# Kernel tuning notes

Hardware: AMD Instinct MI355X
Metric: run time of the kernel (lower is better)

## Reference

```python
import jax, jax.numpy as jnp
import numpy as np

EDGE_WEIGHT = 5.0
LOW, HIGH = 50.0, 150.0          # cv2.Canny thresholds
TG22 = 0.4142135623730951        # tan(22.5 deg)
TG67 = 2.414213562373095         # tan(67.5 deg)


def _conv3(x, k):
    # x: [B,H,W], k: [3,3]; replicate border like cv2.Sobel in Canny
    xp = jnp.pad(x, ((0, 0), (1, 1), (1, 1)), mode='edge')[:, None]
    return jax.lax.conv_general_dilated(xp, k[None, None], (1, 1), 'VALID')[:, 0]


def _dilate(x, k):
    # binary max-pool dilation, zero border (cv2.dilate on 0/255 images)
    return jax.lax.reduce_window(x, 0.0, jax.lax.max, (1, k, k), (1, 1, 1), 'SAME')


def _canny_edge_weight(mask):
    # mask: [B,H,W] float in [0,1] -> per-pixel BCE weight map [B,H,W]
    img = (mask > 0.5).astype(jnp.float32) * 255.0
    kx = jnp.array([[-1., 0., 1.], [-2., 0., 2.], [-1., 0., 1.]], jnp.float32)
    ky = jnp.array([[-1., -2., -1.], [0., 0., 0.], [1., 2., 1.]], jnp.float32)
    gx, gy = _conv3(img, kx), _conv3(img, ky)
    m = jnp.abs(gx) + jnp.abs(gy)  # L1 magnitude (cv2 default L2gradient=False)
    B, H, W = m.shape
    mp = jnp.pad(m, ((0, 0), (1, 1), (1, 1)))  # zero-pad for neighbor lookup
    left, right = mp[:, 1:-1, :-2], mp[:, 1:-1, 2:]
    up, down = mp[:, :-2, 1:-1], mp[:, 2:, 1:-1]
    ul, ur = mp[:, :-2, :-2], mp[:, :-2, 2:]
    dl, dr = mp[:, 2:, :-2], mp[:, 2:, 2:]
    ax, ay = jnp.abs(gx), jnp.abs(gy)
    horiz = ay < ax * TG22
    vert = ay > ax * TG67
    sign_diff = (gx * gy) < 0
    # quantized-direction non-maximum suppression (cv2 tie-breaking: > prev, >= next)
    keep = jnp.where(horiz, (m > left) & (m >= right),
           jnp.where(vert, (m > up) & (m >= down),
           jnp.where(sign_diff, (m > ur) & (m >= dl),
                               (m > ul) & (m >= dr))))
    interior = jnp.zeros((H, W), bool).at[1:-1, 1:-1].set(True)
    cand = keep & (m > LOW) & interior
    weak = cand.astype(jnp.float32)
    strong = (cand & (m > HIGH)).astype(jnp.float32)

    # hysteresis: grow strong edges through weak candidates (8-connectivity)
    def cond(c):
        return c[1]

    def body(c):
        s, _ = c
        ns = jnp.maximum(s, jnp.minimum(weak, _dilate(s, 3)))
        return ns, jnp.any(ns != s)

    strong, _ = jax.lax.while_loop(cond, body, (strong, jnp.array(True)))
    edge_zone = _dilate(strong, 5)  # cv2.dilate(edges, ones(5,5))
    return jnp.where(edge_zone > 0, EDGE_WEIGHT, 1.0)


def setup_inputs() -> dict:
    key = jax.random.key(0)
    k1, k2 = jax.random.split(key)
    B, C, H, W = 16, 1, 1024, 1024
    pred = jax.random.uniform(k1, (B, C, H, W), jnp.float32) * 0.998 + 0.001
    target = (jax.random.uniform(k2, (B, C, H, W), jnp.float32) > 0.7).astype(jnp.float32)
    return {"pred": pred, "target": target}


def reference(pred, target):
    # edge weights from GT mask (detached path, matches .cpu().numpy())
    w = _canny_edge_weight(jax.lax.stop_gradient(target[:, 0]))[:, None]  # [B,1,H,W]
    # BCELoss(reduction='none') with torch's log clamp at -100
    logp = jnp.clip(jnp.log(pred), -100.0)
    log1mp = jnp.clip(jnp.log1p(-pred), -100.0)
    bce = -(target * logp + (1.0 - target) * log1mp)
    return (bce * w).mean()
```

## Files before the change

### kernel.cpp

```cpp
#include <hip/hip_runtime.h>
#include <math.h>


typedef unsigned long long u64;
typedef unsigned int u32;
typedef unsigned short u16;

#define NT 256
#define H_IMG 1024
#define W_IMG 1024
#define WPR 32

constexpr u64 K1 = 0x1111111111111111ULL;
constexpr u64 K7 = 0x7777777777777777ULL;
constexpr u64 K8 = 0x8888888888888888ULL;

__device__ __forceinline__ u64 geq8(u64 x, u64 y) { return ((x | K8) - y) & K8; }
__device__ __forceinline__ u64 gt8(u64 x, u64 y) { return K8 & ~((y | K8) - x); }

__global__ __launch_bounds__(256)
void binarize_kernel(const float* __restrict__ target, u32* __restrict__ packed,
                     int nwords)
{
    int t = blockIdx.x * 256 + threadIdx.x;
    if (t >= nwords) return;
    const float4* src = (const float4*)target + (size_t)t * 8;
    u32 v = 0;
#pragma unroll
    for (int k = 0; k < 8; ++k) {
        float4 f = src[k];
        v |= (f.x > 0.5f ? 1u : 0u) << (4 * k);
        v |= (f.y > 0.5f ? 2u : 0u) << (4 * k);
        v |= (f.z > 0.5f ? 4u : 0u) << (4 * k);
        v |= (f.w > 0.5f ? 8u : 0u) << (4 * k);
    }
    packed[t] = v;
}

__global__ __launch_bounds__(NT)
void edge_loss_kernel(const float* __restrict__ pred,
                      const u32* __restrict__ packed,
                      float* __restrict__ partials)
{
    __shared__ u32 simg[72][11];
    __shared__ u64 mw[70][6];
    __shared__ u64 clw[70][6];
    __shared__ u16 ssw[68][5];
    __shared__ u64 hrow[68];
    __shared__ float wsum[NT / 64];

    const int tid = threadIdx.x;
    const int bz = blockIdx.z;
    const int r0 = blockIdx.y * 64;
    const int c0 = blockIdx.x * 64;
    const float* pimg = pred + (size_t)bz * H_IMG * W_IMG;
    const u32* pb = packed + (size_t)bz * H_IMG * WPR;
    const int W0 = c0 >> 5;

    for (int t = tid; t < 72; t += NT) {
        int r = r0 - 4 + t; r = r < 0 ? 0 : (r > H_IMG - 1 ? H_IMG - 1 : r);
        const u32* prow = pb + r * WPR;
        u32 Bw = prow[W0];
        u32 Cw = prow[W0 + 1];
        u32 Aw = (W0 > 0) ? prow[W0 - 1] : ((Bw & 1u) ? ~0u : 0u);
        u32 Dw = (W0 + 2 < WPR) ? prow[W0 + 2] : ((Cw >> 31) ? ~0u : 0u);
        u64 lo = (u64)(Aw >> 28) | ((u64)Bw << 4) | ((u64)Cw << 36);
        u32 hi = (Cw >> 28) | ((Dw & 0xFu) << 4);
#pragma unroll
        for (int q = 0; q < 9; ++q) {
            u32 x = (q < 8) ? (u32)((lo >> (8 * q)) & 0xFFu) : (hi & 0xFFu);
            x = (x | (x << 12)) & 0x000F000Fu;
            x = (x | (x << 6))  & 0x03030303u;
            x = (x | (x << 3))  & 0x11111111u;
            simg[t][q] = x;
        }
        simg[t][9] = 0; simg[t][10] = 0;
    }
    __syncthreads();

    for (int t = tid; t < 70 * 6; t += NT) {
        int mrow = t / 6, wi = t - mrow * 6;
        if (wi == 5) { mw[mrow][5] = 0; clw[mrow][5] = 0; continue; }
        u64 Lr[3], Cr[3], Rr[3];
#pragma unroll
        for (int k = 0; k < 3; ++k) {
            int ir = mrow + k;
            u32 a0 = simg[ir][2 * wi], a1 = simg[ir][2 * wi + 1], a2 = simg[ir][2 * wi + 2];
            u64 w0 = (u64)a0 | ((u64)a1 << 32);
            Lr[k] = w0;
            Cr[k] = (w0 >> 4) | ((u64)(a2 & 0xFu) << 60);
            Rr[k] = (w0 >> 8) | ((u64)(a2 & 0xFFu) << 56);
        }
        u64 Px = Rr[0] + (Rr[1] << 1) + Rr[2];
        u64 Nx = Lr[0] + (Lr[1] << 1) + Lr[2];
        u64 Py = Lr[2] + (Cr[2] << 1) + Rr[2];
        u64 Ny = Lr[0] + (Cr[0] << 1) + Rr[0];
        u64 Dbx = (Px + K8) - Nx;
        u64 Dby = (Py + K8) - Ny;

        u64 mx = (Dbx >> 3) & K1;
        u64 mfx = (mx << 4) - mx;
        u64 ax = ((Dbx & K7) & mfx) | (((((~Dbx) & K7) + K1)) & ~mfx);
        u64 my = (Dby >> 3) & K1;
        u64 mfy = (my << 4) - my;
        u64 ay = ((Dby & K7) & mfy) | (((((~Dby) & K7) + K1)) & ~mfy);
        u64 m = ax + ay;

        u64 ax0 = ax & K1, ax1b = (ax >> 1) & K1, ax2b = (ax >> 2) & K1;
        u64 ay0 = ay & K1, ay1b = (ay >> 1) & K1, ay2b = (ay >> 2) & K1;
        u64 axnz = ax0 | ax1b | ax2b;
        u64 aynz = ay0 | ay1b | ay2b;
        u64 axe1 = ax0 & ~(ax1b | ax2b);
        u64 aye1 = ay0 & ~(ay1b | ay2b);
        u64 axg3 = ax2b | (ax1b & ax0);
        u64 ayg3 = ay2b | (ay1b & ay0);
        u64 horiz = ((K1 & ~aynz) & axnz) | (aye1 & axg3);
        u64 vert  = ((K1 & ~axnz) & aynz) | (axe1 & ayg3);

        u64 gxp = mx & ((Dbx | (Dbx >> 1) | (Dbx >> 2)) & K1);
        u64 gxn = K1 & ~mx;
        u64 gyp = my & ((Dby | (Dby >> 1) | (Dby >> 2)) & K1);
        u64 gyn = K1 & ~my;
        u64 sd = (gxp & gyn) | (gxn & gyp);

        mw[mrow][wi] = m;
        clw[mrow][wi] = horiz | (vert << 1) | (sd << 2);
    }
    __syncthreads();

    for (int t = tid; t < 68 * 5; t += NT) {
        int srow = t / 5, wi = t - srow * 5;
        u16 outm = 0;
        int rr = r0 - 2 + srow;
        if (rr >= 1 && rr <= H_IMG - 2) {
            int ra = srow, rb = srow + 1, rc = srow + 2;
            u64 a0 = mw[ra][wi], a1 = mw[ra][wi + 1];
            u64 b0 = mw[rb][wi], b1 = mw[rb][wi + 1];
            u64 g0 = mw[rc][wi], g1 = mw[rc][wi + 1];
            u64 U  = (a0 >> 4) | (a1 << 60);
            u64 UL = a0;
            u64 UR = (a0 >> 8) | (a1 << 56);
            u64 M  = (b0 >> 4) | (b1 << 60);
            u64 Lf = b0;
            u64 Rg = (b0 >> 8) | (b1 << 56);
            u64 Dn = (g0 >> 4) | (g1 << 60);
            u64 DL = g0;
            u64 DR = (g0 >> 8) | (g1 << 56);

            u64 q0 = clw[rb][wi], q1 = clw[rb][wi + 1];
            u64 CC = (q0 >> 4) | (q1 << 60);
            u64 H8 = (CC & K1) << 3;
            u64 V8 = ((CC >> 1) & K1) << 3;
            u64 S8 = ((CC >> 2) & K1) << 3;

            u64 kH = gt8(M, Lf) & geq8(M, Rg);
            u64 kV = gt8(M, U)  & geq8(M, Dn);
            u64 kA = gt8(M, UR) & geq8(M, DL);
            u64 kB = gt8(M, UL) & geq8(M, DR);
            u64 nHV = K8 & ~(H8 | V8);
            u64 keep = (H8 & kH) | (V8 & kV) | (nHV & S8 & kA) | (nHV & ~S8 & kB);
            u64 nz = ((M | (M >> 1) | (M >> 2)) & K1) << 3;
            u64 cand = keep & nz;

            int basec = c0 - 2 + 16 * wi;
            int lo = 1 - basec; if (lo < 0) lo = 0;
            int hi = (W_IMG - 2) - basec; if (hi > 15) hi = 15;
            if (lo > hi) cand = 0;
            else cand &= (~0ULL >> ((15 - hi) * 4)) & (~0ULL << (lo * 4));

            u64 x = cand >> 3;
            x = (x | (x >> 3))  & 0x0303030303030303ULL;
            x = (x | (x >> 6))  & 0x000F000F000F000FULL;
            x = (x | (x >> 12)) & 0x000000FF000000FFULL;
            x = (x | (x >> 24));
            outm = (u16)(x & 0xFFFF);
        }
        ssw[srow][wi] = outm;
    }
    __syncthreads();

    for (int t = tid; t < 68; t += NT) {
        u64 lo = (u64)ssw[t][0] | ((u64)ssw[t][1] << 16) |
                 ((u64)ssw[t][2] << 32) | ((u64)ssw[t][3] << 48);
        u64 hib = (u64)(ssw[t][4] & 0xFu);
        u64 acc = lo;
#pragma unroll
        for (int d = 1; d <= 4; ++d)
            acc |= (lo >> d) | (hib << (64 - d));
        hrow[t] = acc;
    }
    __syncthreads();

    float accv = 0.0f;
    {
        int trow = tid >> 2;
        int tcb = (tid & 3) * 16;
        u64 ez64 = hrow[trow] | hrow[trow + 1] | hrow[trow + 2] |
                   hrow[trow + 3] | hrow[trow + 4];
        u64 ezw = ez64 >> tcb;
        int q = (tcb + 4) >> 3;
        u32 ua = simg[trow + 4][q], ub = simg[trow + 4][q + 1], uc = simg[trow + 4][q + 2];
        u64 tb = ((u64)(ua >> 16)) | ((u64)ub << 16) | (((u64)(uc & 0xFFFFu)) << 48);
        const float4* pv4 = (const float4*)(pimg + (size_t)(r0 + trow) * W_IMG + (c0 + tcb));
#pragma unroll
        for (int kk = 0; kk < 4; ++kk) {
            float4 pv = pv4[kk];
            float ps[4] = {pv.x, pv.y, pv.z, pv.w};
#pragma unroll
            for (int cc = 0; cc < 4; ++cc) {
                int k = kk * 4 + cc;
                float p = ps[cc];
                float xx = ((tb >> (4 * k)) & 1) ? p : 1.0f - p;
                float lg = fmaxf(__logf(xx), -100.0f);
                float w = ((ezw >> k) & 1) ? 5.0f : 1.0f;
                accv = fmaf(w, -lg, accv);
            }
        }
    }

    for (int off = 32; off > 0; off >>= 1)
        accv += __shfl_down(accv, off);
    int wid = tid >> 6, lane = tid & 63;
    if (lane == 0) wsum[wid] = accv;
    __syncthreads();
    if (tid == 0) {
        int bi = (blockIdx.z * gridDim.y + blockIdx.y) * gridDim.x + blockIdx.x;
        partials[bi] = wsum[0] + wsum[1] + wsum[2] + wsum[3];
    }
}

__global__ __launch_bounds__(256)
void finalize_kernel(const float* __restrict__ partials, float* __restrict__ out,
                     int nblocks, double invN)
{
    __shared__ double ws[4];
    double s = 0.0;
    for (int i = threadIdx.x; i < nblocks; i += 256) s += (double)partials[i];
    for (int off = 32; off > 0; off >>= 1) s += __shfl_down(s, off);
    int wid = threadIdx.x >> 6, lane = threadIdx.x & 63;
    if (lane == 0) ws[wid] = s;
    __syncthreads();
    if (threadIdx.x == 0) out[0] = (float)((ws[0] + ws[1] + ws[2] + ws[3]) * invN);
}

extern "C" void kernel_launch(void* const* d_in, const int* in_sizes, int n_in,
                              void* d_out, int out_size, void* d_ws, size_t ws_size,
                              hipStream_t stream)
{
    (void)n_in; (void)out_size; (void)ws_size;
    const float* pred   = (const float*)d_in[0];
    const float* target = (const float*)d_in[1];
    const int N = in_sizes[0];
    const int B = N / (H_IMG * W_IMG);

    float* partials = (float*)d_ws;
    u32* packed = (u32*)((char*)d_ws + 16384);
    const int nwords = B * H_IMG * WPR;

    binarize_kernel<<<(nwords + 255) / 256, 256, 0, stream>>>(target, packed, nwords);

    dim3 grid(W_IMG / 64, H_IMG / 64, B);
    int nblocks = (W_IMG / 64) * (H_IMG / 64) * B;
    edge_loss_kernel<<<grid, NT, 0, stream>>>(pred, packed, partials);
    finalize_kernel<<<1, 256, 0, stream>>>(partials, (float*)d_out, nblocks,
                                           1.0 / (double)N);
}
```

Before: 44.83 us.

## Fuse target binarization into edge loss kernel and prefetch pred early

Removes the separate binarize kernel and its packed-bit buffer. Each edge-loss block now reads the float target halo (72x72) directly and thresholds it into the nibble-packed shared image. The pred loads are also issued at kernel start so their latency overlaps the stencil stages. The cost is re-reading halo target floats across neighbouring blocks (about 27% overfetch) and more register pressure from holding pred values.

```diff
diff --git a/kernel.cpp b/kernel.cpp
--- a/kernel.cpp
+++ b/kernel.cpp
@@ -9,7 +9,6 @@
 #define NT 256
 #define H_IMG 1024
 #define W_IMG 1024
-#define WPR 32
 
 constexpr u64 K1 = 0x1111111111111111ULL;
 constexpr u64 K7 = 0x7777777777777777ULL;
@@ -18,28 +17,9 @@
 __device__ __forceinline__ u64 geq8(u64 x, u64 y) { return ((x | K8) - y) & K8; }
 __device__ __forceinline__ u64 gt8(u64 x, u64 y) { return K8 & ~((y | K8) - x); }
 
-__global__ __launch_bounds__(256)
-void binarize_kernel(const float* __restrict__ target, u32* __restrict__ packed,
-                     int nwords)
-{
-    int t = blockIdx.x * 256 + threadIdx.x;
-    if (t >= nwords) return;
-    const float4* src = (const float4*)target + (size_t)t * 8;
-    u32 v = 0;
-#pragma unroll
-    for (int k = 0; k < 8; ++k) {
-        float4 f = src[k];
-        v |= (f.x > 0.5f ? 1u : 0u) << (4 * k);
-        v |= (f.y > 0.5f ? 2u : 0u) << (4 * k);
-        v |= (f.z > 0.5f ? 4u : 0u) << (4 * k);
-        v |= (f.w > 0.5f ? 8u : 0u) << (4 * k);
-    }
-    packed[t] = v;
-}
-
 __global__ __launch_bounds__(NT)
 void edge_loss_kernel(const float* __restrict__ pred,
-                      const u32* __restrict__ packed,
+                      const float* __restrict__ target,
                       float* __restrict__ partials)
 {
     __shared__ u32 simg[72][11];
@@ -54,27 +34,42 @@
     const int r0 = blockIdx.y * 64;
     const int c0 = blockIdx.x * 64;
     const float* pimg = pred + (size_t)bz * H_IMG * W_IMG;
-    const u32* pb = packed + (size_t)bz * H_IMG * WPR;
-    const int W0 = c0 >> 5;
-
-    for (int t = tid; t < 72; t += NT) {
-        int r = r0 - 4 + t; r = r < 0 ? 0 : (r > H_IMG - 1 ? H_IMG - 1 : r);
-        const u32* prow = pb + r * WPR;
-        u32 Bw = prow[W0];
-        u32 Cw = prow[W0 + 1];
-        u32 Aw = (W0 > 0) ? prow[W0 - 1] : ((Bw & 1u) ? ~0u : 0u);
-        u32 Dw = (W0 + 2 < WPR) ? prow[W0 + 2] : ((Cw >> 31) ? ~0u : 0u);
-        u64 lo = (u64)(Aw >> 28) | ((u64)Bw << 4) | ((u64)Cw << 36);
-        u32 hi = (Cw >> 28) | ((Dw & 0xFu) << 4);
-#pragma unroll
-        for (int q = 0; q < 9; ++q) {
-            u32 x = (q < 8) ? (u32)((lo >> (8 * q)) & 0xFFu) : (hi & 0xFFu);
-            x = (x | (x << 12)) & 0x000F000Fu;
-            x = (x | (x << 6))  & 0x03030303u;
-            x = (x | (x << 3))  & 0x11111111u;
-            simg[t][q] = x;
-        }
-        simg[t][9] = 0; simg[t][10] = 0;
+    const float* timg = target + (size_t)bz * H_IMG * W_IMG;
+
+    const int trow = tid >> 2;
+    const int tcb = (tid & 3) * 16;
+    const float4* pv4 = (const float4*)(pimg + (size_t)(r0 + trow) * W_IMG + (c0 + tcb));
+    float4 pf[4];
+#pragma unroll
+    for (int k = 0; k < 4; ++k) pf[k] = pv4[k];
+
+    for (int t = tid; t < 72 * 9; t += NT) {
+        int tr = t / 9, q = t - tr * 9;
+        int r = r0 - 4 + tr; r = r < 0 ? 0 : (r > H_IMG - 1 ? H_IMG - 1 : r);
+        const float* rowp = timg + (size_t)r * W_IMG;
+        int cbase = c0 - 4 + 8 * q;
+        u32 x;
+        if (cbase >= 0 && cbase + 7 <= W_IMG - 1) {
+            float4 f0 = *(const float4*)(rowp + cbase);
+            float4 f1 = *(const float4*)(rowp + cbase + 4);
+            x  = (f0.x > 0.5f ? 0x1u        : 0u)
+               | (f0.y > 0.5f ? 0x10u       : 0u)
+               | (f0.z > 0.5f ? 0x100u      : 0u)
+               | (f0.w > 0.5f ? 0x1000u     : 0u)
+               | (f1.x > 0.5f ? 0x10000u    : 0u)
+               | (f1.y > 0.5f ? 0x100000u   : 0u)
+               | (f1.z > 0.5f ? 0x1000000u  : 0u)
+               | (f1.w > 0.5f ? 0x10000000u : 0u);
+        } else {
+            x = 0;
+#pragma unroll
+            for (int k = 0; k < 8; ++k) {
+                int c = cbase + k; c = c < 0 ? 0 : (c > W_IMG - 1 ? W_IMG - 1 : c);
+                x |= (rowp[c] > 0.5f ? 1u : 0u) << (4 * k);
+            }
+        }
+        simg[tr][q] = x;
+        if (q == 0) { simg[tr][9] = 0; simg[tr][10] = 0; }
     }
     __syncthreads();
 
@@ -193,18 +188,15 @@
 
     float accv = 0.0f;
     {
-        int trow = tid >> 2;
-        int tcb = (tid & 3) * 16;
         u64 ez64 = hrow[trow] | hrow[trow + 1] | hrow[trow + 2] |
                    hrow[trow + 3] | hrow[trow + 4];
         u64 ezw = ez64 >> tcb;
         int q = (tcb + 4) >> 3;
         u32 ua = simg[trow + 4][q], ub = simg[trow + 4][q + 1], uc = simg[trow + 4][q + 2];
         u64 tb = ((u64)(ua >> 16)) | ((u64)ub << 16) | (((u64)(uc & 0xFFFFu)) << 48);
-        const float4* pv4 = (const float4*)(pimg + (size_t)(r0 + trow) * W_IMG + (c0 + tcb));
 #pragma unroll
         for (int kk = 0; kk < 4; ++kk) {
-            float4 pv = pv4[kk];
+            float4 pv = pf[kk];
             float ps[4] = {pv.x, pv.y, pv.z, pv.w};
 #pragma unroll
             for (int cc = 0; cc < 4; ++cc) {
@@ -254,14 +246,10 @@
     const int B = N / (H_IMG * W_IMG);
 
     float* partials = (float*)d_ws;
-    u32* packed = (u32*)((char*)d_ws + 16384);
-    const int nwords = B * H_IMG * WPR;
-
-    binarize_kernel<<<(nwords + 255) / 256, 256, 0, stream>>>(target, packed, nwords);
 
     dim3 grid(W_IMG / 64, H_IMG / 64, B);
     int nblocks = (W_IMG / 64) * (H_IMG / 64) * B;
-    edge_loss_kernel<<<grid, NT, 0, stream>>>(pred, packed, partials);
+    edge_loss_kernel<<<grid, NT, 0, stream>>>(pred, target, partials);
     finalize_kernel<<<1, 256, 0, stream>>>(partials, (float*)d_out, nblocks,
                                            1.0 / (double)N);
 }
```

Measured after the change: 48.50 us. 1.08x slower.

## Prefetch pred early and fold final reduction into last-block atomic counter

Applied to the files above, without the earlier changes.

Issues the per-thread pred float4 loads at kernel start so their latency overlaps the bit-packed Canny/hysteresis work in shared memory. It also removes the separate finalize kernel: each block bumps an atomic counter after writing its partial, and the last block sums all partials and writes the mean. This trades one kernel launch for a memset, an atomic and fences, and holds 16 extra registers per thread across the edge computation, which may hurt occupancy.

```diff
diff --git a/kernel.cpp b/kernel.cpp
--- a/kernel.cpp
+++ b/kernel.cpp
@@ -40,7 +40,10 @@
 __global__ __launch_bounds__(NT)
 void edge_loss_kernel(const float* __restrict__ pred,
                       const u32* __restrict__ packed,
-                      float* __restrict__ partials)
+                      float* __restrict__ partials,
+                      u32* __restrict__ done_ctr,
+                      float* __restrict__ out,
+                      int nblocks, double invN)
 {
     __shared__ u32 simg[72][11];
     __shared__ u64 mw[70][6];
@@ -48,6 +51,8 @@
     __shared__ u16 ssw[68][5];
     __shared__ u64 hrow[68];
     __shared__ float wsum[NT / 64];
+    __shared__ double dsum[NT / 64];
+    __shared__ u32 lastf;
 
     const int tid = threadIdx.x;
     const int bz = blockIdx.z;
@@ -56,6 +61,13 @@
     const float* pimg = pred + (size_t)bz * H_IMG * W_IMG;
     const u32* pb = packed + (size_t)bz * H_IMG * WPR;
     const int W0 = c0 >> 5;
+
+    const int trow = tid >> 2;
+    const int tcb = (tid & 3) * 16;
+    const float4* pv4 = (const float4*)(pimg + (size_t)(r0 + trow) * W_IMG + (c0 + tcb));
+    float4 pf[4];
+#pragma unroll
+    for (int k = 0; k < 4; ++k) pf[k] = pv4[k];
 
     for (int t = tid; t < 72; t += NT) {
         int r = r0 - 4 + t; r = r < 0 ? 0 : (r > H_IMG - 1 ? H_IMG - 1 : r);
@@ -193,18 +205,15 @@
 
     float accv = 0.0f;
     {
-        int trow = tid >> 2;
-        int tcb = (tid & 3) * 16;
         u64 ez64 = hrow[trow] | hrow[trow + 1] | hrow[trow + 2] |
                    hrow[trow + 3] | hrow[trow + 4];
         u64 ezw = ez64 >> tcb;
         int q = (tcb + 4) >> 3;
         u32 ua = simg[trow + 4][q], ub = simg[trow + 4][q + 1], uc = simg[trow + 4][q + 2];
         u64 tb = ((u64)(ua >> 16)) | ((u64)ub << 16) | (((u64)(uc & 0xFFFFu)) << 48);
-        const float4* pv4 = (const float4*)(pimg + (size_t)(r0 + trow) * W_IMG + (c0 + tcb));
 #pragma unroll
         for (int kk = 0; kk < 4; ++kk) {
-            float4 pv = pv4[kk];
+            float4 pv = pf[kk];
             float ps[4] = {pv.x, pv.y, pv.z, pv.w};
 #pragma unroll
             for (int cc = 0; cc < 4; ++cc) {
@@ -226,21 +235,26 @@
     if (tid == 0) {
         int bi = (blockIdx.z * gridDim.y + blockIdx.y) * gridDim.x + blockIdx.x;
         partials[bi] = wsum[0] + wsum[1] + wsum[2] + wsum[3];
-    }
-}
-
-__global__ __launch_bounds__(256)
-void finalize_kernel(const float* __restrict__ partials, float* __restrict__ out,
-                     int nblocks, double invN)
-{
-    __shared__ double ws[4];
-    double s = 0.0;
-    for (int i = threadIdx.x; i < nblocks; i += 256) s += (double)partials[i];
-    for (int off = 32; off > 0; off >>= 1) s += __shfl_down(s, off);
-    int wid = threadIdx.x >> 6, lane = threadIdx.x & 63;
-    if (lane == 0) ws[wid] = s;
-    __syncthreads();
-    if (threadIdx.x == 0) out[0] = (float)((ws[0] + ws[1] + ws[2] + ws[3]) * invN);
+        __threadfence();
+        u32 r = atomicAdd(done_ctr, 1u);
+        lastf = (r == (u32)(nblocks - 1)) ? 1u : 0u;
+    }
+    __syncthreads();
+
+    if (lastf) {
+        __threadfence();
+        double s = 0.0;
+        for (int i = tid; i < nblocks; i += NT)
+            s += (double)((volatile float*)partials)[i];
+        for (int off = 32; off > 0; off >>= 1)
+            s += __shfl_down(s, off);
+        if (lane == 0) dsum[wid] = s;
+        __syncthreads();
+        if (tid == 0) {
+            out[0] = (float)((dsum[0] + dsum[1] + dsum[2] + dsum[3]) * invN);
+            *done_ctr = 0;
+        }
+    }
 }
 
 extern "C" void kernel_launch(void* const* d_in, const int* in_sizes, int n_in,
@@ -255,13 +269,16 @@
 
     float* partials = (float*)d_ws;
     u32* packed = (u32*)((char*)d_ws + 16384);
+    u32* done_ctr = (u32*)((char*)d_ws + 16384 + (size_t)2 * 1024 * 1024);
     const int nwords = B * H_IMG * WPR;
+
+    hipMemsetAsync(done_ctr, 0, 4, stream);
 
     binarize_kernel<<<(nwords + 255) / 256, 256, 0, stream>>>(target, packed, nwords);
 
     dim3 grid(W_IMG / 64, H_IMG / 64, B);
     int nblocks = (W_IMG / 64) * (H_IMG / 64) * B;
-    edge_loss_kernel<<<grid, NT, 0, stream>>>(pred, packed, partials);
-    finalize_kernel<<<1, 256, 0, stream>>>(partials, (float*)d_out, nblocks,
-                                           1.0 / (double)N);
+    edge_loss_kernel<<<grid, NT, 0, stream>>>(pred, packed, partials, done_ctr,
+                                              (float*)d_out, nblocks,
+                                              1.0 / (double)N);
 }
```

Result: slower. 131.0 us (+192.3%).
